# Performance work log

Hardware: AMD Instinct MI355X
Metric: run time of the kernel (lower is better)

Reference implementation:

```python
import jax, jax.numpy as jnp
import numpy as np

K = 3  # s_kernel_size = max_graph_distance + 1

def setup_inputs() -> dict:
    key = jax.random.key(0)
    k1, k2, k3, k4, k5 = jax.random.split(key, 5)
    N, C_IN, T, V = 64, 64, 300, 25
    C_OUT = 128
    x = jax.random.normal(k1, (N, C_IN, T, V), dtype=jnp.float32)
    A = jax.random.uniform(k2, (K, V, V), dtype=jnp.float32)
    # 1x1 Conv2d(in=64, out=128*3) -> weight [384, 64] (kernel dims squeezed), bias [384]
    weight = jax.random.normal(k3, (C_OUT * K, C_IN), dtype=jnp.float32) * 0.05
    bias = jax.random.normal(k4, (C_OUT * K,), dtype=jnp.float32) * 0.05
    index = jax.random.randint(k5, (V,), 0, V, dtype=jnp.int64)
    return {"x": x, "A": A, "weight": weight, "bias": bias, "index": index}

def reference(x, A, weight, bias, index):
    n, c_in, t, v = x.shape
    kc = weight.shape[0]
    c_out = kc // K
    # 1x1 conv == channel GEMM: [n, kc, t, v]
    y = jnp.einsum('nitv,oi->notv', x, weight) + bias[None, :, None, None]
    # split kernel dim: [n, K, c_out, t, v]
    y = y.reshape(n, K, c_out, t, v)
    # gather adjacency rows: A[:K, index, :] -> [K, v, w]
    A_sel = A[:K, index, :]
    # contract over k and w (v shared between y and A_sel)
    out = jnp.einsum('nkctv,kvw->nctv', y, A_sel)
    return out
```

## Files before the change

### kernel.cpp

```cpp
#include <hip/hip_runtime.h>
#include <cstddef>
#include <cstdint>

#define N_DIM 64
#define C_IN 64
#define C_OUT 128
#define T_DIM 300
#define V_DIM 25
#define TVTOT (T_DIM * V_DIM)
#define TILE 64
#define NTILE ((TVTOT + TILE - 1) / TILE)
#define KTOT 192
#define NKS (KTOT / 32)
#define ROWB 384
#define WFRAG_BYTES (8 * NKS * 64 * 8 * 2)

typedef unsigned int uint32;
typedef unsigned short ushort16;
typedef float f32x4 __attribute__((ext_vector_type(4)));
typedef short bf16x8 __attribute__((ext_vector_type(8)));
typedef uint32 u32x4 __attribute__((ext_vector_type(4)));

__device__ __forceinline__ ushort16 f2bf(float f) {
  uint32 u = __float_as_uint(f);
  u = (u + 0x7FFFu + ((u >> 16) & 1u)) >> 16;
  return (ushort16)u;
}
__device__ __forceinline__ uint32 pack2(float a, float b) {
  return (uint32)f2bf(a) | ((uint32)f2bf(b) << 16);
}

__global__ __launch_bounds__(384)
void sgc_prep(const float* __restrict__ A, const float* __restrict__ W,
              const int* __restrict__ index,
              ushort16* __restrict__ Wfrag, float* __restrict__ sS4) {
  const int m = blockIdx.x;
  const int tid = threadIdx.x;

  if (m == 0 && tid < 3 * V_DIM) {
    const int k = tid / V_DIM;
    const int v = tid - k * V_DIM;
    const int idx = index[v];
    float s = 0.f;
    #pragma unroll
    for (int w = 0; w < V_DIM; ++w) s += A[(k * V_DIM + idx) * V_DIM + w];
    sS4[v * 4 + k] = s;
    if (k == 0) sS4[v * 4 + 3] = 0.f;
  }

  const int ks = tid >> 6;
  const int lane = tid & 63;
  const int c = (m << 4) + (lane & 15);
  const int kk0 = (ks << 5) + ((lane >> 4) << 3);
  const int k = kk0 >> 6;
  const int i0 = kk0 & 63;
  const float* wrow = W + (size_t)(k * C_OUT + c) * C_IN + i0;
  u32x4 w4;
  #pragma unroll
  for (int p = 0; p < 4; ++p)
    w4[p] = pack2(wrow[2 * p], wrow[2 * p + 1]);
  *(u32x4*)((ushort16*)Wfrag + (((m * NKS + ks) * 64 + lane) << 3)) = w4;
}

__global__ __launch_bounds__(256)
void sgc_main(const float* __restrict__ x, const ushort16* __restrict__ Wfrag,
              const float* __restrict__ sS4, const float* __restrict__ bias,
              float* __restrict__ out) {
  __shared__ __align__(16) ushort16 xs[TILE * (ROWB / 2)];

  const int tid = threadIdx.x;
  const int wv = tid >> 6;
  const int lane = tid & 63;
  const int tile = blockIdx.x;
  const int n = blockIdx.y;
  const int tv0 = tile * TILE;

  bf16x8 afr[2][NKS];
  #pragma unroll
  for (int m2 = 0; m2 < 2; ++m2)
    #pragma unroll
    for (int ks = 0; ks < NKS; ++ks)
      afr[m2][ks] = *(const bf16x8*)((const ushort16*)Wfrag +
                        ((((2 * wv + m2) * NKS + ks) * 64 + lane) << 3));

  const int tvg = tv0 + lane;
  const bool tvok = tvg < TVTOT;
  const int vstage = tvok ? (tvg % V_DIM) : 0;
  const f32x4 sv = *(const f32x4*)(sS4 + 4 * vstage);
  float xv[16];
  {
    const float* xp = x + ((size_t)n * C_IN + wv * 16) * TVTOT + tvg;
    if (tvok) {
      #pragma unroll
      for (int j = 0; j < 16; ++j) xv[j] = xp[j * TVTOT];
    } else {
      #pragma unroll
      for (int j = 0; j < 16; ++j) xv[j] = 0.f;
    }
  }
  #pragma unroll
  for (int k = 0; k < 3; ++k) {
    const float sk = sv[k];
    u32x4 w0, w1;
    #pragma unroll
    for (int p = 0; p < 4; ++p) {
      w0[p] = pack2(xv[2 * p] * sk, xv[2 * p + 1] * sk);
      w1[p] = pack2(xv[8 + 2 * p] * sk, xv[9 + 2 * p] * sk);
    }
    const int sb = k * 8 + 2 * wv;
    char* rowp = (char*)xs + lane * ROWB;
    *(u32x4*)(rowp + ((sb ^ (lane & 7)) << 4)) = w0;
    *(u32x4*)(rowp + (((sb + 1) ^ (lane & 7)) << 4)) = w1;
  }
  __syncthreads();

  f32x4 acc[2][4];
  #pragma unroll
  for (int m2 = 0; m2 < 2; ++m2)
    #pragma unroll
    for (int f = 0; f < 4; ++f) acc[m2][f] = (f32x4){0.f, 0.f, 0.f, 0.f};

  #pragma unroll
  for (int ks = 0; ks < NKS; ++ks) {
    bf16x8 bfr[4];
    #pragma unroll
    for (int f = 0; f < 4; ++f) {
      const int col = 16 * f + (lane & 15);
      const int sl = (4 * ks + (lane >> 4)) ^ (lane & 7);
      bfr[f] = *(const bf16x8*)((const char*)xs + col * ROWB + (sl << 4));
    }
    #pragma unroll
    for (int m2 = 0; m2 < 2; ++m2)
      #pragma unroll
      for (int f = 0; f < 4; ++f)
        acc[m2][f] = __builtin_amdgcn_mfma_f32_16x16x32_bf16(
            afr[m2][ks], bfr[f], acc[m2][f], 0, 0, 0);
  }

  const int rg = (lane >> 4) << 2;
  f32x4 bfr3[2][3];
  #pragma unroll
  for (int m2 = 0; m2 < 2; ++m2) {
    const int c0 = 32 * wv + 16 * m2 + rg;
    #pragma unroll
    for (int k = 0; k < 3; ++k)
      bfr3[m2][k] = *(const f32x4*)(bias + k * C_OUT + c0);
  }
  float* outn = out + (size_t)n * C_OUT * TVTOT;
  #pragma unroll
  for (int f = 0; f < 4; ++f) {
    const int tvc = tv0 + 16 * f + (lane & 15);
    if (tvc < TVTOT) {
      const int v = tvc % V_DIM;
      const f32x4 s2 = *(const f32x4*)(sS4 + 4 * v);
      #pragma unroll
      for (int m2 = 0; m2 < 2; ++m2) {
        const int c0 = 32 * wv + 16 * m2 + rg;
        const f32x4 badd =
            s2[0] * bfr3[m2][0] + s2[1] * bfr3[m2][1] + s2[2] * bfr3[m2][2];
        const f32x4 r = acc[m2][f] + badd;
        #pragma unroll
        for (int q = 0; q < 4; ++q)
          outn[(size_t)(c0 + q) * TVTOT + tvc] = r[q];
      }
    }
  }
}

extern "C" void kernel_launch(void* const* d_in, const int* in_sizes, int n_in,
                              void* d_out, int out_size, void* d_ws, size_t ws_size,
                              hipStream_t stream) {
  const float* x      = (const float*)d_in[0];
  const float* A      = (const float*)d_in[1];
  const float* weight = (const float*)d_in[2];
  const float* bias   = (const float*)d_in[3];
  const int*   index  = (const int*)d_in[4];
  float* out = (float*)d_out;

  ushort16* Wfrag = (ushort16*)d_ws;
  float* sS4 = (float*)((char*)d_ws + WFRAG_BYTES);

  sgc_prep<<<dim3(8), dim3(384), 0, stream>>>(A, weight, index, Wfrag, sS4);
  sgc_main<<<dim3(NTILE, N_DIM), dim3(256), 0, stream>>>(x, Wfrag, sS4, bias, out);
}
```

Measured before the change: 387.6 us.

## Make main kernel persistent with register prefetch of next x tile

Replaces the one-block-per-tile grid with a persistent grid of 1888 blocks. Each block loops over work items and prefetches the next tile's x values into registers while the current tile's MFMA runs, so weight fragments are loaded once per block. It also precomputes an effective per-vertex bias table in the prep kernel, uses the hardware v_cvt_pk_bf16_f32 instruction for packing, and splits the prep work across more blocks. The costs are extra register pressure from the double-buffered x, an additional barrier per iteration, and a grid size hardcoded to the device.

```diff
diff --git a/kernel.cpp b/kernel.cpp
--- a/kernel.cpp
+++ b/kernel.cpp
@@ -10,10 +10,13 @@
 #define TVTOT (T_DIM * V_DIM)
 #define TILE 64
 #define NTILE ((TVTOT + TILE - 1) / TILE)
-#define KTOT 192
-#define NKS (KTOT / 32)
+#define TOTAL (N_DIM * NTILE)
+#define NBLK 1888
+#define NKS 6
 #define ROWB 384
 #define WFRAG_BYTES (8 * NKS * 64 * 8 * 2)
+#define SS4_OFF WFRAG_BYTES
+#define BEFF_OFF (WFRAG_BYTES + 1024)
 
 typedef unsigned int uint32;
 typedef unsigned short ushort16;
@@ -29,141 +32,172 @@
 __device__ __forceinline__ uint32 pack2(float a, float b) {
   return (uint32)f2bf(a) | ((uint32)f2bf(b) << 16);
 }
-
-__global__ __launch_bounds__(384)
+__device__ __forceinline__ uint32 cvt_pk(float lo, float hi) {
+  uint32 r;
+  asm("v_cvt_pk_bf16_f32 %0, %1, %2" : "=v"(r) : "v"(lo), "v"(hi));
+  return r;
+}
+
+__global__ __launch_bounds__(128)
 void sgc_prep(const float* __restrict__ A, const float* __restrict__ W,
-              const int* __restrict__ index,
-              ushort16* __restrict__ Wfrag, float* __restrict__ sS4) {
-  const int m = blockIdx.x;
+              const float* __restrict__ bias, const int* __restrict__ index,
+              ushort16* __restrict__ Wfrag, float* __restrict__ sS4,
+              float* __restrict__ beff) {
+  const int bid = blockIdx.x;
   const int tid = threadIdx.x;
-
-  if (m == 0 && tid < 3 * V_DIM) {
-    const int k = tid / V_DIM;
-    const int v = tid - k * V_DIM;
-    const int idx = index[v];
-    float s = 0.f;
-    #pragma unroll
-    for (int w = 0; w < V_DIM; ++w) s += A[(k * V_DIM + idx) * V_DIM + w];
-    sS4[v * 4 + k] = s;
-    if (k == 0) sS4[v * 4 + 3] = 0.f;
+  if (bid < 24) {
+    const int m = bid / 3;
+    const int ks = (bid % 3) * 2 + (tid >> 6);
+    const int lane = tid & 63;
+    const int c = (m << 4) + (lane & 15);
+    const int kk0 = (ks << 5) + ((lane >> 4) << 3);
+    const int k = kk0 >> 6;
+    const int i0 = kk0 & 63;
+    const float* wrow = W + (size_t)(k * C_OUT + c) * C_IN + i0;
+    u32x4 w4;
+    #pragma unroll
+    for (int p = 0; p < 4; ++p)
+      w4[p] = pack2(wrow[2 * p], wrow[2 * p + 1]);
+    *(u32x4*)(Wfrag + (((m * NKS + ks) * 64 + lane) << 3)) = w4;
+  } else {
+    __shared__ float sl[3 * V_DIM];
+    if (tid < 3 * V_DIM) {
+      const int k = tid / V_DIM;
+      const int v = tid - k * V_DIM;
+      const int idx = index[v];
+      float s = 0.f;
+      #pragma unroll
+      for (int w = 0; w < V_DIM; ++w) s += A[(k * V_DIM + idx) * V_DIM + w];
+      sl[k * V_DIM + v] = s;
+      sS4[v * 4 + k] = s;
+      if (k == 0) sS4[v * 4 + 3] = 0.f;
+    }
+    __syncthreads();
+    const float b0 = bias[tid];
+    const float b1 = bias[C_OUT + tid];
+    const float b2 = bias[2 * C_OUT + tid];
+    #pragma unroll
+    for (int v = 0; v < V_DIM; ++v)
+      beff[v * C_OUT + tid] =
+          sl[v] * b0 + sl[V_DIM + v] * b1 + sl[2 * V_DIM + v] * b2;
   }
-
-  const int ks = tid >> 6;
-  const int lane = tid & 63;
-  const int c = (m << 4) + (lane & 15);
-  const int kk0 = (ks << 5) + ((lane >> 4) << 3);
-  const int k = kk0 >> 6;
-  const int i0 = kk0 & 63;
-  const float* wrow = W + (size_t)(k * C_OUT + c) * C_IN + i0;
-  u32x4 w4;
-  #pragma unroll
-  for (int p = 0; p < 4; ++p)
-    w4[p] = pack2(wrow[2 * p], wrow[2 * p + 1]);
-  *(u32x4*)((ushort16*)Wfrag + (((m * NKS + ks) * 64 + lane) << 3)) = w4;
-}
-
-__global__ __launch_bounds__(256)
+}
+
+__device__ __forceinline__ void load_x(const float* __restrict__ x, int wi,
+                                       int wv, int lane, float xv[16]) {
+  const int n = wi / NTILE;
+  const int tile = wi - n * NTILE;
+  const int tvg = tile * TILE + lane;
+  if (tvg < TVTOT) {
+    const float* xp = x + ((size_t)n * C_IN + wv * 16) * TVTOT + tvg;
+    #pragma unroll
+    for (int j = 0; j < 16; ++j) xv[j] = xp[j * TVTOT];
+  } else {
+    #pragma unroll
+    for (int j = 0; j < 16; ++j) xv[j] = 0.f;
+  }
+}
+
+__global__ __launch_bounds__(256, 3)
 void sgc_main(const float* __restrict__ x, const ushort16* __restrict__ Wfrag,
-              const float* __restrict__ sS4, const float* __restrict__ bias,
+              const float* __restrict__ sS4, const float* __restrict__ beff,
               float* __restrict__ out) {
   __shared__ __align__(16) ushort16 xs[TILE * (ROWB / 2)];
 
   const int tid = threadIdx.x;
   const int wv = tid >> 6;
   const int lane = tid & 63;
-  const int tile = blockIdx.x;
-  const int n = blockIdx.y;
-  const int tv0 = tile * TILE;
 
   bf16x8 afr[2][NKS];
   #pragma unroll
   for (int m2 = 0; m2 < 2; ++m2)
     #pragma unroll
     for (int ks = 0; ks < NKS; ++ks)
-      afr[m2][ks] = *(const bf16x8*)((const ushort16*)Wfrag +
+      afr[m2][ks] = *(const bf16x8*)(Wfrag +
                         ((((2 * wv + m2) * NKS + ks) * 64 + lane) << 3));
 
-  const int tvg = tv0 + lane;
-  const bool tvok = tvg < TVTOT;
-  const int vstage = tvok ? (tvg % V_DIM) : 0;
-  const f32x4 sv = *(const f32x4*)(sS4 + 4 * vstage);
+  int wi = blockIdx.x;
   float xv[16];
-  {
-    const float* xp = x + ((size_t)n * C_IN + wv * 16) * TVTOT + tvg;
-    if (tvok) {
-      #pragma unroll
-      for (int j = 0; j < 16; ++j) xv[j] = xp[j * TVTOT];
+  load_x(x, wi, wv, lane, xv);
+
+  for (; wi < TOTAL; wi += NBLK) {
+    const int n = wi / NTILE;
+    const int tile = wi - n * NTILE;
+    const int tv0 = tile * TILE;
+    const int tvg = tv0 + lane;
+    const int vstage = (tvg < TVTOT) ? (tvg % V_DIM) : 0;
+    const f32x4 sv = *(const f32x4*)(sS4 + 4 * vstage);
+
+    #pragma unroll
+    for (int k = 0; k < 3; ++k) {
+      const float sk = sv[k];
+      u32x4 w0, w1;
+      #pragma unroll
+      for (int p = 0; p < 4; ++p) {
+        w0[p] = cvt_pk(xv[2 * p] * sk, xv[2 * p + 1] * sk);
+        w1[p] = cvt_pk(xv[8 + 2 * p] * sk, xv[9 + 2 * p] * sk);
+      }
+      const int sb = k * 8 + 2 * wv;
+      char* rowp = (char*)xs + lane * ROWB;
+      *(u32x4*)(rowp + ((sb ^ (lane & 7)) << 4)) = w0;
+      *(u32x4*)(rowp + (((sb + 1) ^ (lane & 7)) << 4)) = w1;
+    }
+
+    float xv2[16];
+    const int wn = wi + NBLK;
+    if (wn < TOTAL) {
+      load_x(x, wn, wv, lane, xv2);
     } else {
       #pragma unroll
-      for (int j = 0; j < 16; ++j) xv[j] = 0.f;
-    }
-  }
-  #pragma unroll
-  for (int k = 0; k < 3; ++k) {
-    const float sk = sv[k];
-    u32x4 w0, w1;
-    #pragma unroll
-    for (int p = 0; p < 4; ++p) {
-      w0[p] = pack2(xv[2 * p] * sk, xv[2 * p + 1] * sk);
-      w1[p] = pack2(xv[8 + 2 * p] * sk, xv[9 + 2 * p] * sk);
-    }
-    const int sb = k * 8 + 2 * wv;
-    char* rowp = (char*)xs + lane * ROWB;
-    *(u32x4*)(rowp + ((sb ^ (lane & 7)) << 4)) = w0;
-    *(u32x4*)(rowp + (((sb + 1) ^ (lane & 7)) << 4)) = w1;
-  }
-  __syncthreads();
-
-  f32x4 acc[2][4];
-  #pragma unroll
-  for (int m2 = 0; m2 < 2; ++m2)
-    #pragma unroll
-    for (int f = 0; f < 4; ++f) acc[m2][f] = (f32x4){0.f, 0.f, 0.f, 0.f};
-
-  #pragma unroll
-  for (int ks = 0; ks < NKS; ++ks) {
-    bf16x8 bfr[4];
+      for (int j = 0; j < 16; ++j) xv2[j] = 0.f;
+    }
+    __syncthreads();
+
+    f32x4 acc[2][4];
+    #pragma unroll
+    for (int m2 = 0; m2 < 2; ++m2)
+      #pragma unroll
+      for (int f = 0; f < 4; ++f) acc[m2][f] = (f32x4){0.f, 0.f, 0.f, 0.f};
+
+    #pragma unroll
+    for (int ks = 0; ks < NKS; ++ks) {
+      bf16x8 bfr[4];
+      #pragma unroll
+      for (int f = 0; f < 4; ++f) {
+        const int col = 16 * f + (lane & 15);
+        const int sl = (4 * ks + (lane >> 4)) ^ (lane & 7);
+        bfr[f] = *(const bf16x8*)((const char*)xs + col * ROWB + (sl << 4));
+      }
+      #pragma unroll
+      for (int m2 = 0; m2 < 2; ++m2)
+        #pragma unroll
+        for (int f = 0; f < 4; ++f)
+          acc[m2][f] = __builtin_amdgcn_mfma_f32_16x16x32_bf16(
+              afr[m2][ks], bfr[f], acc[m2][f], 0, 0, 0);
+    }
+    __syncthreads();
+
+    const int rg = (lane >> 4) << 2;
+    float* outn = out + (size_t)n * C_OUT * TVTOT;
     #pragma unroll
     for (int f = 0; f < 4; ++f) {
-      const int col = 16 * f + (lane & 15);
-      const int sl = (4 * ks + (lane >> 4)) ^ (lane & 7);
-      bfr[f] = *(const bf16x8*)((const char*)xs + col * ROWB + (sl << 4));
-    }
-    #pragma unroll
-    for (int m2 = 0; m2 < 2; ++m2)
-      #pragma unroll
-      for (int f = 0; f < 4; ++f)
-        acc[m2][f] = __builtin_amdgcn_mfma_f32_16x16x32_bf16(
-            afr[m2][ks], bfr[f], acc[m2][f], 0, 0, 0);
-  }
-
-  const int rg = (lane >> 4) << 2;
-  f32x4 bfr3[2][3];
-  #pragma unroll
-  for (int m2 = 0; m2 < 2; ++m2) {
-    const int c0 = 32 * wv + 16 * m2 + rg;
-    #pragma unroll
-    for (int k = 0; k < 3; ++k)
-      bfr3[m2][k] = *(const f32x4*)(bias + k * C_OUT + c0);
-  }
-  float* outn = out + (size_t)n * C_OUT * TVTOT;
-  #pragma unroll
-  for (int f = 0; f < 4; ++f) {
-    const int tvc = tv0 + 16 * f + (lane & 15);
-    if (tvc < TVTOT) {
-      const int v = tvc % V_DIM;
-      const f32x4 s2 = *(const f32x4*)(sS4 + 4 * v);
-      #pragma unroll
-      for (int m2 = 0; m2 < 2; ++m2) {
-        const int c0 = 32 * wv + 16 * m2 + rg;
-        const f32x4 badd =
-            s2[0] * bfr3[m2][0] + s2[1] * bfr3[m2][1] + s2[2] * bfr3[m2][2];
-        const f32x4 r = acc[m2][f] + badd;
+      const int tvc = tv0 + 16 * f + (lane & 15);
+      if (tvc < TVTOT) {
+        const int v = tvc % V_DIM;
         #pragma unroll
-        for (int q = 0; q < 4; ++q)
-          outn[(size_t)(c0 + q) * TVTOT + tvc] = r[q];
+        for (int m2 = 0; m2 < 2; ++m2) {
+          const int c0 = 32 * wv + 16 * m2 + rg;
+          const f32x4 b4 = *(const f32x4*)(beff + v * C_OUT + c0);
+          const f32x4 r = acc[m2][f] + b4;
+          #pragma unroll
+          for (int q = 0; q < 4; ++q)
+            outn[(size_t)(c0 + q) * TVTOT + tvc] = r[q];
+        }
       }
     }
+
+    #pragma unroll
+    for (int j = 0; j < 16; ++j) xv[j] = xv2[j];
   }
 }
 
@@ -178,8 +212,9 @@
   float* out = (float*)d_out;
 
   ushort16* Wfrag = (ushort16*)d_ws;
-  float* sS4 = (float*)((char*)d_ws + WFRAG_BYTES);
-
-  sgc_prep<<<dim3(8), dim3(384), 0, stream>>>(A, weight, index, Wfrag, sS4);
-  sgc_main<<<dim3(NTILE, N_DIM), dim3(256), 0, stream>>>(x, Wfrag, sS4, bias, out);
-}
+  float* sS4  = (float*)((char*)d_ws + SS4_OFF);
+  float* beff = (float*)((char*)d_ws + BEFF_OFF);
+
+  sgc_prep<<<dim3(25), dim3(128), 0, stream>>>(A, weight, bias, index, Wfrag, sS4, beff);
+  sgc_main<<<dim3(NBLK), dim3(256), 0, stream>>>(x, Wfrag, sS4, beff, out);
+}
```

After: 415.4 us. 7.2% more time.
